# Performance work log

Measured on AMD Instinct MI355X. Metric: run time of the kernel, lower is better.

## Reference

```python
import jax, jax.numpy as jnp
import numpy as np

I_, J_, D_IN, D_H = 100, 8, 768, 64
N_NODES, N_HE, N_INC, N_CELLS, VOCAB = 160000, 320000, 1600000, 800, 30000
BN_EPS = 1e-5


def setup_inputs() -> dict:
    key = jax.random.key(0)
    ks = jax.random.split(key, 20)
    w = lambda k, s: jax.random.normal(k, s, jnp.float32) * 0.05
    inp = {}
    inp['x'] = jax.random.normal(ks[0], (I_, J_, D_IN), jnp.float32)
    inp['node_tokens'] = jax.random.randint(ks[1], (N_NODES,), 0, VOCAB)
    inp['inc_node'] = jax.random.randint(ks[2], (N_INC,), 0, N_NODES)
    inp['inc_hedge'] = jnp.sort(jax.random.randint(ks[3], (N_INC,), 0, N_HE))
    inp['node2cell'] = jnp.sort(jax.random.randint(ks[4], (N_NODES,), 0, N_CELLS))
    inp['vac_emb'] = w(ks[5], (VOCAB, D_IN))
    inp['fhi_w'] = w(ks[6], (D_IN, D_H)); inp['fhi_b'] = jnp.zeros((D_H,), jnp.float32)
    inp['fin_w'] = w(ks[7], (D_IN, D_H)); inp['fin_b'] = jnp.zeros((D_H,), jnp.float32)
    inp['th1'] = w(ks[8], (D_H, D_H)); inp['b1'] = jnp.zeros((D_H,), jnp.float32)
    inp['th2'] = w(ks[9], (D_H, D_H)); inp['b2'] = jnp.zeros((D_H,), jnp.float32)
    for li, k in zip((1, 2, 3), (ks[10], ks[11], ks[12])):
        inp[f'wc{li}'] = w(k, (D_H, D_H, 3))
        inp[f'bc{li}'] = jnp.zeros((D_H,), jnp.float32)
        inp[f'g{li}'] = jnp.ones((D_H,), jnp.float32)
        inp[f'be{li}'] = jnp.zeros((D_H,), jnp.float32)
        inp[f'm{li}'] = jnp.zeros((D_H,), jnp.float32)
        inp[f'v{li}'] = jnp.ones((D_H,), jnp.float32)
    inp['fct_w'] = w(ks[13], (D_H, D_H)); inp['fct_b'] = jnp.zeros((D_H,), jnp.float32)
    return inp


def _inv_safe(c):
    return jnp.where(c > 0, 1.0 / jnp.maximum(c, 1.0), 0.0)


def _hconv(xf, inc_node, inc_hedge, theta, bias):
    # PyG HypergraphConv (no attention): D^{-1} H W B^{-1} H^T (X Theta) + bias
    xt = xf @ theta                                        # [N, D]
    ones = jnp.ones((inc_node.shape[0],), xt.dtype)
    deg_e = jax.ops.segment_sum(ones, inc_hedge, N_HE)     # B_e
    he = jax.ops.segment_sum(xt[inc_node], inc_hedge, N_HE) * _inv_safe(deg_e)[:, None]
    deg_v = jax.ops.segment_sum(ones, inc_node, N_NODES)   # D_v
    out = jax.ops.segment_sum(he[inc_hedge], inc_node, N_NODES) * _inv_safe(deg_v)[:, None]
    return out + bias


def _conv_bn(h, wc, bc, g, be, m, v):
    # Conv1d(k=3, pad=1) -> ReLU -> BatchNorm1d (inference stats); dropout is eval-mode identity
    h = jax.lax.conv_general_dilated(h, wc, (1,), [(1, 1)],
                                     dimension_numbers=('NCH', 'OIH', 'NCH')) + bc[None, :, None]
    h = jax.nn.relu(h)
    return (h - m[None, :, None]) * (g[None, :, None] / jnp.sqrt(v[None, :, None] + BN_EPS)) + be[None, :, None]


def _forward(x, node_tokens, inc_node, inc_hedge, node2cell, vac_emb, fhi_w, fhi_b,
             fin_w, fin_b, th1, b1, th2, b2, wc1, bc1, g1, be1, m1, v1,
             wc2, bc2, g2, be2, m2, v2, wc3, bc3, g3, be3, m3, v3, fct_w, fct_b):
    # x = fin(x)
    x0 = jnp.einsum('ijd,dh->ijh', x, fin_w) + fin_b       # [100, 8, 64]
    # node_features = fhi(graph_embedding[graph.x])  (gather-dominated)
    nf = vac_emb[node_tokens] @ fhi_w + fhi_b              # [N, 64]
    # two HypergraphConv layers with residuals (eval-mode dropout = identity)
    h1 = jax.nn.relu(_hconv(nf, inc_node, inc_hedge, th1, b1)) + nf
    gx = jax.nn.relu(_hconv(h1, inc_node, inc_hedge, th2, b2)) + nf
    # per-graph mean + max pooling (graph.batch is all-zero per graph => one vector per cell)
    cnt = jax.ops.segment_sum(jnp.ones((N_NODES,), gx.dtype), node2cell, N_CELLS)
    mean_p = jax.ops.segment_sum(gx, node2cell, N_CELLS) * _inv_safe(cnt)[:, None]
    max_p = jax.ops.segment_max(gx, node2cell, N_CELLS)
    max_p = jnp.where(cnt[:, None] > 0, max_p, 0.0)
    cell_emb = 0.5 * (mean_p + max_p)                      # [800, 64]
    x_upd = x0 + 0.3 * cell_emb.reshape(I_, J_, D_H)       # x[i,j] += 0.3*graph_emb
    h = jnp.transpose(x_upd, (0, 2, 1))                    # [100, 64, 8]
    h = _conv_bn(h, wc1, bc1, g1, be1, m1, v1)
    h = _conv_bn(h, wc2, bc2, g2, be2, m2, v2)
    h = _conv_bn(h, wc3, bc3, g3, be3, m3, v3)
    out2 = jnp.mean(h, axis=2) @ fct_w + fct_b             # [100, 64]
    return x_upd, out2


def reference(x, node_tokens, inc_node, inc_hedge, node2cell, vac_emb, fhi_w, fhi_b,
              fin_w, fin_b, th1, b1, th2, b2, wc1, bc1, g1, be1, m1, v1,
              wc2, bc2, g2, be2, m2, v2, wc3, bc3, g3, be3, m3, v3, fct_w, fct_b):
    return _forward(x, node_tokens, inc_node, inc_hedge, node2cell, vac_emb, fhi_w, fhi_b,
                    fin_w, fin_b, th1, b1, th2, b2, wc1, bc1, g1, be1, m1, v1,
                    wc2, bc2, g2, be2, m2, v2, wc3, bc3, g3, be3, m3, v3, fct_w, fct_b)
```

## Files before the change

### kernel.cpp

```cpp
#include <hip/hip_runtime.h>
#include <hip/hip_bf16.h>
#include <cstdint>
#include <cstddef>

#define I_      100
#define J_      8
#define D_IN    768
#define D_H     64
#define N_NODES 160000
#define N_HE    320000
#define N_INC   1600000
#define N_CELLS 800
#define VOCAB   30000

#define NRANGE   256
#define NPR      625
#define SLAB     8192
#define NCHUNK   1000
#define EPB      (N_INC / NCHUNK)

typedef unsigned short u16;
using short8 = __attribute__((ext_vector_type(8))) short;
using f32x4  = __attribute__((ext_vector_type(4))) float;

__device__ __forceinline__ float bf2f(u16 u) {
    union { uint32_t i; float f; } x; x.i = ((uint32_t)u) << 16; return x.f;
}
__device__ __forceinline__ u16 f2bf(float f) {
    union { float f; uint32_t i; } x; x.f = f;
    uint32_t b = x.i;
    b += 0x7FFFu + ((b >> 16) & 1u);
    return (u16)(b >> 16);
}
__device__ __forceinline__ float lo_bf(uint32_t u) {
    union { uint32_t i; float f; } x; x.i = u << 16; return x.f;
}
__device__ __forceinline__ float hi_bf(uint32_t u) {
    union { uint32_t i; float f; } x; x.i = u & 0xFFFF0000u; return x.f;
}
__device__ __forceinline__ uint32_t pack_bf2(float a, float b) {
    return (uint32_t)f2bf(a) | ((uint32_t)f2bf(b) << 16);
}

#define G_OFF_HE   (N_INC / 256)
#define G_OFF_CELL (N_NODES / 256)
#define G_CONV_BIG ((D_IN * 64) / 256)
#define G_CONV_SM  ((64 * 64) / 256)
#define G_KA       NCHUNK
#define G_KB1      256
#define G_KC       NCHUNK
#define G_KD       256
#define G_PGEMM    ((VOCAB + 63) / 64)
#define G_XT       (N_NODES / 64)
#define G_X0       ((I_ * J_ + 63) / 64)
#define G_HEDGE    (N_HE / 32)
#define G_NODE     (N_NODES / 32)
#define G_NXT      (N_NODES / 32)

__device__ __forceinline__ void dev_offsets(int bid, const int* __restrict__ sorted,
                                            int n, int nbins, int* __restrict__ off) {
    int i = bid * 256 + threadIdx.x;
    if (i >= n) return;
    int cur = sorted[i];
    int prev = (i == 0) ? -1 : sorted[i - 1];
    for (int b = prev + 1; b <= cur; ++b) off[b] = i;
    if (i == n - 1) {
        for (int b = cur + 1; b <= nbins; ++b) off[b] = n;
    }
}

__device__ __forceinline__ void dev_convT(int bid, const float* __restrict__ B,
                                          u16* __restrict__ Bt, int K) {
    int g = bid * 256 + threadIdx.x;
    if (g >= K * 64) return;
    int k = g >> 6, n = g & 63;
    Bt[(size_t)n * K + k] = f2bf(B[g]);
}

__device__ __forceinline__ void dev_ka(int bid, const int* __restrict__ inc_node,
                                       int* __restrict__ counts, int* __restrict__ lds) {
    int tid = threadIdx.x;
    lds[tid] = 0;
    __syncthreads();
    int s = bid * EPB, e = s + EPB;
    for (int i = s + tid; i < e; i += 256)
        atomicAdd(&lds[(unsigned)inc_node[i] / NPR], 1);
    __syncthreads();
    counts[bid * NRANGE + tid] = lds[tid];
}

__device__ __forceinline__ void dev_kb1(int r, const int* __restrict__ counts,
                                        int* __restrict__ chunk_off,
                                        int* __restrict__ range_total,
                                        int* __restrict__ lds) {
    int tid = threadIdx.x;
    int c0 = tid * 4;
    int v0 = (c0     < NCHUNK) ? counts[(c0    ) * NRANGE + r] : 0;
    int v1 = (c0 + 1 < NCHUNK) ? counts[(c0 + 1) * NRANGE + r] : 0;
    int v2 = (c0 + 2 < NCHUNK) ? counts[(c0 + 2) * NRANGE + r] : 0;
    int v3 = (c0 + 3 < NCHUNK) ? counts[(c0 + 3) * NRANGE + r] : 0;
    int s = v0 + v1 + v2 + v3;
    lds[tid] = s;
    __syncthreads();
    #pragma unroll
    for (int d = 1; d < 256; d <<= 1) {
        int t = (tid >= d) ? lds[tid - d] : 0;
        __syncthreads();
        lds[tid] += t;
        __syncthreads();
    }
    int run = lds[tid] - s;
    if (c0     < NCHUNK) { chunk_off[(c0    ) * NRANGE + r] = run; run += v0; }
    if (c0 + 1 < NCHUNK) { chunk_off[(c0 + 1) * NRANGE + r] = run; run += v1; }
    if (c0 + 2 < NCHUNK) { chunk_off[(c0 + 2) * NRANGE + r] = run; run += v2; }
    if (c0 + 3 < NCHUNK) { chunk_off[(c0 + 3) * NRANGE + r] = run; run += v3; }
    if (tid == 255) range_total[r] = lds[255];
}

__device__ __forceinline__ void dev_kc(int bid, const int* __restrict__ inc_node,
                                       const int* __restrict__ inc_hedge,
                                       const int* __restrict__ chunk_off,
                                       int2* __restrict__ bucket, int* __restrict__ lds) {
    int tid = threadIdx.x;
    int* co  = lds;
    int* cur = lds + 256;
    co[tid]  = tid * SLAB + chunk_off[bid * NRANGE + tid];
    cur[tid] = 0;
    __syncthreads();
    int s = bid * EPB, e = s + EPB;
    for (int i = s + tid; i < e; i += 256) {
        int v = inc_node[i];
        int h = inc_hedge[i];
        int rg = (unsigned)v / NPR;
        int rank = atomicAdd(&cur[rg], 1);
        bucket[co[rg] + rank] = make_int2(v, h);
    }
}

__device__ __forceinline__ void dev_kd(int r, const int2* __restrict__ bucket,
                                       const int* __restrict__ range_total,
                                       int* __restrict__ node_off, int* __restrict__ node_deg,
                                       int* __restrict__ csr, int* __restrict__ lds) {
    int tid = threadIdx.x;
    int* hist = lds;
    int* tsum = lds + 768;
    int* cur  = lds + 1024;
    for (int i = tid; i < 768; i += 256) { hist[i] = 0; cur[i] = 0; }
    __syncthreads();
    int lo = r * NPR;
    int pb = r * SLAB;
    int pe = pb + range_total[r];
    for (int i = pb + tid; i < pe; i += 256)
        atomicAdd(&hist[bucket[i].x - lo], 1);
    __syncthreads();
    int b3 = tid * 3;
    int a0 = hist[b3], a1 = hist[b3 + 1], a2 = hist[b3 + 2];
    int s = a0 + a1 + a2;
    tsum[tid] = s;
    __syncthreads();
    #pragma unroll
    for (int d = 1; d < 256; d <<= 1) {
        int t = (tid >= d) ? tsum[tid - d] : 0;
        __syncthreads();
        tsum[tid] += t;
        __syncthreads();
    }
    int excl = tsum[tid] - s;
    hist[b3]     = excl;
    hist[b3 + 1] = excl + a0;
    hist[b3 + 2] = excl + a0 + a1;
    __syncthreads();
    for (int v = tid; v < NPR; v += 256) {
        int h0 = hist[v];
        node_off[lo + v] = pb + h0;
        node_deg[lo + v] = hist[v + 1] - h0;
    }
    for (int i = pb + tid; i < pe; i += 256) {
        int2 p = bucket[i];
        int l = p.x - lo;
        int k = atomicAdd(&cur[l], 1);
        csr[pb + hist[l] + k] = p.y;
    }
}

template <int BF16_OUT, int GATHER, int KK>
__device__ __forceinline__ void dev_gemm_direct(int wid, const float* __restrict__ A,
                                                const int* __restrict__ tok,
                                                const u16* __restrict__ Bt,
                                                const float* __restrict__ bias,
                                                void* __restrict__ C, int M) {
    int lane = threadIdx.x & 63;
    int m16 = lane & 15, q = lane >> 4;
    int base = wid << 4;
    if (base >= M) return;
    int row = base + m16;
    const float* arow = GATHER ? (A + ((size_t)tok[row] << 6))
                               : (A + (size_t)row * KK);

    f32x4 acc0 = {0.f, 0.f, 0.f, 0.f};
    f32x4 acc1 = {0.f, 0.f, 0.f, 0.f};
    f32x4 acc2 = {0.f, 0.f, 0.f, 0.f};
    f32x4 acc3 = {0.f, 0.f, 0.f, 0.f};

    #pragma unroll 2
    for (int kt = 0; kt < KK; kt += 32) {
        const float* ap = arow + kt + q * 8;
        float4 av0 = *reinterpret_cast<const float4*>(ap);
        float4 av1 = *reinterpret_cast<const float4*>(ap + 4);
        short8 a;
        a[0] = (short)f2bf(av0.x); a[1] = (short)f2bf(av0.y);
        a[2] = (short)f2bf(av0.z); a[3] = (short)f2bf(av0.w);
        a[4] = (short)f2bf(av1.x); a[5] = (short)f2bf(av1.y);
        a[6] = (short)f2bf(av1.z); a[7] = (short)f2bf(av1.w);
        const u16* bp = Bt + (size_t)m16 * KK + kt + q * 8;
        short8 b0 = *reinterpret_cast<const short8*>(bp);
        short8 b1 = *reinterpret_cast<const short8*>(bp + (size_t)16 * KK);
        short8 b2 = *reinterpret_cast<const short8*>(bp + (size_t)32 * KK);
        short8 b3 = *reinterpret_cast<const short8*>(bp + (size_t)48 * KK);
        acc0 = __builtin_amdgcn_mfma_f32_16x16x32_bf16(a, b0, acc0, 0, 0, 0);
        acc1 = __builtin_amdgcn_mfma_f32_16x16x32_bf16(a, b1, acc1, 0, 0, 0);
        acc2 = __builtin_amdgcn_mfma_f32_16x16x32_bf16(a, b2, acc2, 0, 0, 0);
        acc3 = __builtin_amdgcn_mfma_f32_16x16x32_bf16(a, b3, acc3, 0, 0, 0);
    }

    f32x4 accs[4] = {acc0, acc1, acc2, acc3};
    #pragma unroll
    for (int r = 0; r < 4; ++r) {
        int gr = base + q * 4 + r;
        #pragma unroll
        for (int j = 0; j < 4; ++j) {
            int col = j * 16 + m16;
            float v = accs[j][r];
            if (!BF16_OUT) v += bias[col];
            if (BF16_OUT)
                ((u16*)C)[(size_t)gr * 64 + col] = f2bf(v);
            else
                ((float*)C)[(size_t)gr * 64 + col] = v;
        }
    }
}

__device__ __forceinline__ void dev_hedge_sum(int bid, const int* __restrict__ inc_node,
                                              const int* __restrict__ he_off,
                                              const u16* __restrict__ xt,
                                              u16* __restrict__ he) {
    int w = (bid * 256 + (int)threadIdx.x) >> 6;
    int lane = threadIdx.x & 63;
    int sub = lane >> 3;
    int c8 = (lane & 7) << 3;
    int hedge = w * 8 + sub;
    if (hedge >= N_HE) return;
    int s = he_off[hedge], e = he_off[hedge + 1];

    float a0 = 0.f, a1 = 0.f, a2 = 0.f, a3 = 0.f;
    float a4 = 0.f, a5 = 0.f, a6 = 0.f, a7 = 0.f;
    float b0 = 0.f, b1 = 0.f, b2 = 0.f, b3 = 0.f;
    float b4 = 0.f, b5 = 0.f, b6 = 0.f, b7 = 0.f;

    int j = s;
    if ((e - s) & 1) {
        uint4 d = *reinterpret_cast<const uint4*>(xt + (((size_t)inc_node[j]) << 6) + c8);
        a0 += lo_bf(d.x); a1 += hi_bf(d.x);
        a2 += lo_bf(d.y); a3 += hi_bf(d.y);
        a4 += lo_bf(d.z); a5 += hi_bf(d.z);
        a6 += lo_bf(d.w); a7 += hi_bf(d.w);
        ++j;
    }
    int i0 = 0, i1 = 0;
    if (j < e) { i0 = inc_node[j]; i1 = inc_node[j + 1]; }
    for (; j < e; j += 2) {
        int c0 = i0, c1 = i1;
        if (j + 2 < e) { i0 = inc_node[j + 2]; i1 = inc_node[j + 3]; }
        uint4 d0 = *reinterpret_cast<const uint4*>(xt + (((size_t)c0) << 6) + c8);
        uint4 d1 = *reinterpret_cast<const uint4*>(xt + (((size_t)c1) << 6) + c8);
        a0 += lo_bf(d0.x); a1 += hi_bf(d0.x);
        a2 += lo_bf(d0.y); a3 += hi_bf(d0.y);
        a4 += lo_bf(d0.z); a5 += hi_bf(d0.z);
        a6 += lo_bf(d0.w); a7 += hi_bf(d0.w);
        b0 += lo_bf(d1.x); b1 += hi_bf(d1.x);
        b2 += lo_bf(d1.y); b3 += hi_bf(d1.y);
        b4 += lo_bf(d1.z); b5 += hi_bf(d1.z);
        b6 += lo_bf(d1.w); b7 += hi_bf(d1.w);
    }
    a0 += b0; a1 += b1; a2 += b2; a3 += b3;
    a4 += b4; a5 += b5; a6 += b6; a7 += b7;

    float inv = (e > s) ? 1.f / (float)(e - s) : 0.f;
    uint4 o;
    o.x = pack_bf2(a0 * inv, a1 * inv);
    o.y = pack_bf2(a2 * inv, a3 * inv);
    o.z = pack_bf2(a4 * inv, a5 * inv);
    o.w = pack_bf2(a6 * inv, a7 * inv);
    *reinterpret_cast<uint4*>(he + (((size_t)hedge) << 6) + c8) = o;
}

__device__ __forceinline__ void dev_node_core(int node, const int* __restrict__ csr,
                                              const int* __restrict__ node_off,
                                              const int* __restrict__ node_deg,
                                              const u16* __restrict__ he,
                                              const float* __restrict__ bias,
                                              const float* __restrict__ P,
                                              const int* __restrict__ tok,
                                              int c8, float* __restrict__ o) {
    int s = node_off[node];
    int e = s + node_deg[node];

    float a0 = 0.f, a1 = 0.f, a2 = 0.f, a3 = 0.f;
    float a4 = 0.f, a5 = 0.f, a6 = 0.f, a7 = 0.f;
    float b0 = 0.f, b1 = 0.f, b2 = 0.f, b3 = 0.f;
    float b4 = 0.f, b5 = 0.f, b6 = 0.f, b7 = 0.f;

    int j = s;
    if ((e - s) & 1) {
        uint4 d = *reinterpret_cast<const uint4*>(he + (((size_t)csr[j]) << 6) + c8);
        a0 += lo_bf(d.x); a1 += hi_bf(d.x);
        a2 += lo_bf(d.y); a3 += hi_bf(d.y);
        a4 += lo_bf(d.z); a5 += hi_bf(d.z);
        a6 += lo_bf(d.w); a7 += hi_bf(d.w);
        ++j;
    }
    int i0 = 0, i1 = 0;
    if (j < e) { i0 = csr[j]; i1 = csr[j + 1]; }
    for (; j < e; j += 2) {
        int c0 = i0, c1 = i1;
        if (j + 2 < e) { i0 = csr[j + 2]; i1 = csr[j + 3]; }
        uint4 d0 = *reinterpret_cast<const uint4*>(he + (((size_t)c0) << 6) + c8);
        uint4 d1 = *reinterpret_cast<const uint4*>(he + (((size_t)c1) << 6) + c8);
        a0 += lo_bf(d0.x); a1 += hi_bf(d0.x);
        a2 += lo_bf(d0.y); a3 += hi_bf(d0.y);
        a4 += lo_bf(d0.z); a5 += hi_bf(d0.z);
        a6 += lo_bf(d0.w); a7 += hi_bf(d0.w);
        b0 += lo_bf(d1.x); b1 += hi_bf(d1.x);
        b2 += lo_bf(d1.y); b3 += hi_bf(d1.y);
        b4 += lo_bf(d1.z); b5 += hi_bf(d1.z);
        b6 += lo_bf(d1.w); b7 += hi_bf(d1.w);
    }
    a0 += b0; a1 += b1; a2 += b2; a3 += b3;
    a4 += b4; a5 += b5; a6 += b6; a7 += b7;

    float inv = (e > s) ? 1.f / (float)(e - s) : 0.f;
    const float* nfp = P + (((size_t)tok[node]) << 6) + c8;
    float4 nv0 = *reinterpret_cast<const float4*>(nfp);
    float4 nv1 = *reinterpret_cast<const float4*>(nfp + 4);
    o[0] = fmaxf(fmaf(a0, inv, bias[c8 + 0]), 0.f) + nv0.x;
    o[1] = fmaxf(fmaf(a1, inv, bias[c8 + 1]), 0.f) + nv0.y;
    o[2] = fmaxf(fmaf(a2, inv, bias[c8 + 2]), 0.f) + nv0.z;
    o[3] = fmaxf(fmaf(a3, inv, bias[c8 + 3]), 0.f) + nv0.w;
    o[4] = fmaxf(fmaf(a4, inv, bias[c8 + 4]), 0.f) + nv1.x;
    o[5] = fmaxf(fmaf(a5, inv, bias[c8 + 5]), 0.f) + nv1.y;
    o[6] = fmaxf(fmaf(a6, inv, bias[c8 + 6]), 0.f) + nv1.z;
    o[7] = fmaxf(fmaf(a7, inv, bias[c8 + 7]), 0.f) + nv1.w;
}

__global__ __launch_bounds__(256) void k_node_xt(const int* __restrict__ csr,
                                                 const int* __restrict__ node_off,
                                                 const int* __restrict__ node_deg,
                                                 const u16* __restrict__ he,
                                                 const float* __restrict__ bias,
                                                 const float* __restrict__ P,
                                                 const int* __restrict__ tok,
                                                 const u16* __restrict__ Bt,
                                                 u16* __restrict__ xt) {
    __shared__ u16 h1s[32][72];
    int tid = threadIdx.x;
    int w = tid >> 6;
    int lane = tid & 63;
    int sub = lane >> 3;
    int c8 = (lane & 7) << 3;
    int rowib = w * 8 + sub;
    int node = blockIdx.x * 32 + rowib;

    float o[8];
    dev_node_core(node, csr, node_off, node_deg, he, bias, P, tok, c8, o);

    uint4 pk;
    pk.x = pack_bf2(o[0], o[1]);
    pk.y = pack_bf2(o[2], o[3]);
    pk.z = pack_bf2(o[4], o[5]);
    pk.w = pack_bf2(o[6], o[7]);
    *reinterpret_cast<uint4*>(&h1s[rowib][c8]) = pk;
    __syncthreads();

    if (w < 2) {
        int m16 = lane & 15, q = lane >> 4;
        int base = w * 16;
        f32x4 acc0 = {0.f, 0.f, 0.f, 0.f};
        f32x4 acc1 = {0.f, 0.f, 0.f, 0.f};
        f32x4 acc2 = {0.f, 0.f, 0.f, 0.f};
        f32x4 acc3 = {0.f, 0.f, 0.f, 0.f};
        #pragma unroll
        for (int kt = 0; kt < 64; kt += 32) {
            short8 a = *reinterpret_cast<const short8*>(&h1s[base + m16][kt + q * 8]);
            const u16* bp = Bt + (size_t)m16 * 64 + kt + q * 8;
            short8 b0 = *reinterpret_cast<const short8*>(bp);
            short8 b1 = *reinterpret_cast<const short8*>(bp + (size_t)16 * 64);
            short8 b2 = *reinterpret_cast<const short8*>(bp + (size_t)32 * 64);
            short8 b3 = *reinterpret_cast<const short8*>(bp + (size_t)48 * 64);
            acc0 = __builtin_amdgcn_mfma_f32_16x16x32_bf16(a, b0, acc0, 0, 0, 0);
            acc1 = __builtin_amdgcn_mfma_f32_16x16x32_bf16(a, b1, acc1, 0, 0, 0);
            acc2 = __builtin_amdgcn_mfma_f32_16x16x32_bf16(a, b2, acc2, 0, 0, 0);
            acc3 = __builtin_amdgcn_mfma_f32_16x16x32_bf16(a, b3, acc3, 0, 0, 0);
        }
        f32x4 accs[4] = {acc0, acc1, acc2, acc3};
        #pragma unroll
        for (int r = 0; r < 4; ++r) {
            int gr = blockIdx.x * 32 + base + q * 4 + r;
            #pragma unroll
            for (int jj = 0; jj < 4; ++jj) {
                int col = jj * 16 + m16;
                xt[(size_t)gr * 64 + col] = f2bf(accs[jj][r]);
            }
        }
    }
}

__global__ __launch_bounds__(256) void k_node_sum(const int* __restrict__ csr,
                                                  const int* __restrict__ node_off,
                                                  const int* __restrict__ node_deg,
                                                  const u16* __restrict__ he,
                                                  const float* __restrict__ bias,
                                                  const float* __restrict__ P,
                                                  const int* __restrict__ tok,
                                                  float* __restrict__ out) {
    int w = (blockIdx.x * 256 + (int)threadIdx.x) >> 6;
    int lane = threadIdx.x & 63;
    int sub = lane >> 3;
    int c8 = (lane & 7) << 3;
    int node = w * 8 + sub;
    if (node >= N_NODES) return;
    float o[8];
    dev_node_core(node, csr, node_off, node_deg, he, bias, P, tok, c8, o);
    float* op = out + (((size_t)node) << 6) + c8;
    float4 o0 = make_float4(o[0], o[1], o[2], o[3]);
    float4 o1 = make_float4(o[4], o[5], o[6], o[7]);
    *reinterpret_cast<float4*>(op) = o0;
    *reinterpret_cast<float4*>(op + 4) = o1;
}

__global__ __launch_bounds__(256) void k_p0(const float* __restrict__ fhi_w,
                                            const float* __restrict__ fin_w,
                                            const float* __restrict__ th1,
                                            const float* __restrict__ th2,
                                            u16* __restrict__ Bt_fhi, u16* __restrict__ Bt_fin,
                                            u16* __restrict__ Bt_th1, u16* __restrict__ Bt_th2,
                                            const int* __restrict__ inc_node,
                                            int* __restrict__ counts) {
    __shared__ int lds[256];
    int bid = blockIdx.x;
    if (bid < G_KA) { dev_ka(bid, inc_node, counts, lds); return; }
    bid -= G_KA;
    if (bid < G_CONV_BIG) { dev_convT(bid, fhi_w, Bt_fhi, D_IN); return; }
    bid -= G_CONV_BIG;
    if (bid < G_CONV_BIG) { dev_convT(bid, fin_w, Bt_fin, D_IN); return; }
    bid -= G_CONV_BIG;
    if (bid < G_CONV_SM) { dev_convT(bid, th1, Bt_th1, 64); return; }
    bid -= G_CONV_SM;
    dev_convT(bid, th2, Bt_th2, 64);
}

__global__ __launch_bounds__(256) void k_p1(const float* __restrict__ vac_emb,
                                            const u16* __restrict__ Bt_fhi,
                                            const float* __restrict__ fhi_b, float* __restrict__ P,
                                            const int* __restrict__ counts,
                                            int* __restrict__ chunk_off, int* __restrict__ range_total,
                                            const int* __restrict__ inc_hedge,
                                            const int* __restrict__ node2cell,
                                            int* __restrict__ he_off, int* __restrict__ cell_off) {
    __shared__ int lds[256];
    int bid = blockIdx.x;
    if (bid < G_KB1) { dev_kb1(bid, counts, chunk_off, range_total, lds); return; }
    bid -= G_KB1;
    if (bid < G_PGEMM) {
        int wid = bid * 4 + ((int)threadIdx.x >> 6);
        dev_gemm_direct<0, 0, D_IN>(wid, vac_emb, nullptr, Bt_fhi, fhi_b, P, VOCAB);
        return;
    }
    bid -= G_PGEMM;
    if (bid < G_OFF_HE) { dev_offsets(bid, inc_hedge, N_INC, N_HE, he_off); return; }
    bid -= G_OFF_HE;
    dev_offsets(bid, node2cell, N_NODES, N_CELLS, cell_off);
}

__global__ __launch_bounds__(256) void k_p2(const float* __restrict__ P,
                                            const int* __restrict__ tok,
                                            const u16* __restrict__ Bt_th1, u16* __restrict__ xt,
                                            const float* __restrict__ x, const u16* __restrict__ Bt_fin,
                                            const float* __restrict__ fin_b, float* __restrict__ x0,
                                            const int* __restrict__ inc_node,
                                            const int* __restrict__ inc_hedge,
                                            const int* __restrict__ chunk_off,
                                            int2* __restrict__ bucket) {
    __shared__ int lds[512];
    int bid = blockIdx.x;
    if (bid < G_KC) { dev_kc(bid, inc_node, inc_hedge, chunk_off, bucket, lds); return; }
    bid -= G_KC;
    if (bid < G_XT) {
        int wid = bid * 4 + ((int)threadIdx.x >> 6);
        dev_gemm_direct<1, 1, 64>(wid, P, tok, Bt_th1, nullptr, xt, N_NODES);
        return;
    }
    bid -= G_XT;
    {
        int wid = bid * 4 + ((int)threadIdx.x >> 6);
        dev_gemm_direct<0, 0, D_IN>(wid, x, nullptr, Bt_fin, fin_b, x0, I_ * J_);
    }
}

__global__ __launch_bounds__(256) void k_p3(const int* __restrict__ inc_node,
                                            const int* __restrict__ he_off,
                                            const u16* __restrict__ xt, u16* __restrict__ he,
                                            const int2* __restrict__ bucket,
                                            const int* __restrict__ range_total,
                                            int* __restrict__ node_off, int* __restrict__ node_deg,
                                            int* __restrict__ csr) {
    __shared__ int lds[1792];
    int bid = blockIdx.x;
    if (bid < G_KD) { dev_kd(bid, bucket, range_total, node_off, node_deg, csr, lds); return; }
    bid -= G_KD;
    dev_hedge_sum(bid, inc_node, he_off, xt, he);
}

__global__ __launch_bounds__(256) void k_hedge_sum(const int* __restrict__ inc_node,
                                                   const int* __restrict__ he_off,
                                                   const u16* __restrict__ xt,
                                                   u16* __restrict__ he) {
    dev_hedge_sum(blockIdx.x, inc_node, he_off, xt, he);
}

__global__ __launch_bounds__(256) void k_pool(const float* __restrict__ gx,
                                              const int* __restrict__ cell_off,
                                              const float* __restrict__ x0,
                                              float* __restrict__ out1) {
    __shared__ float ssum[4][64];
    __shared__ float smax[4][64];
    int c = blockIdx.x;
    int lane = threadIdx.x & 63;
    int w = threadIdx.x >> 6;
    int s = cell_off[c], e = cell_off[c + 1];
    float sum = 0.f, mx = -INFINITY;
    for (int n = s + w; n < e; n += 4) {
        float v = gx[((size_t)n << 6) + lane];
        sum += v;
        mx = fmaxf(mx, v);
    }
    ssum[w][lane] = sum;
    smax[w][lane] = mx;
    __syncthreads();
    if (w == 0) {
        sum = ssum[0][lane] + ssum[1][lane] + ssum[2][lane] + ssum[3][lane];
        mx = fmaxf(fmaxf(smax[0][lane], smax[1][lane]), fmaxf(smax[2][lane], smax[3][lane]));
        int cnt = e - s;
        float mean = (cnt > 0) ? sum / (float)cnt : 0.f;
        float mp = (cnt > 0) ? mx : 0.f;
        float ce = 0.5f * (mean + mp);
        out1[((size_t)c << 6) + lane] = x0[((size_t)c << 6) + lane] + 0.3f * ce;
    }
}

__global__ __launch_bounds__(256) void k_tcn(
    const float* __restrict__ xu,
    const float* __restrict__ wc1, const float* __restrict__ bc1, const float* __restrict__ g1,
    const float* __restrict__ be1, const float* __restrict__ m1, const float* __restrict__ v1,
    const float* __restrict__ wc2, const float* __restrict__ bc2, const float* __restrict__ g2,
    const float* __restrict__ be2, const float* __restrict__ m2, const float* __restrict__ v2,
    const float* __restrict__ wc3, const float* __restrict__ bc3, const float* __restrict__ g3,
    const float* __restrict__ be3, const float* __restrict__ m3, const float* __restrict__ v3,
    const float* __restrict__ fct_w, const float* __restrict__ fct_b,
    float* __restrict__ out2) {
    __shared__ float w_lds[64 * 64 * 3];
    __shared__ float hA[64][10];
    __shared__ float hB[64][10];
    __shared__ float mo[64];

    int n = blockIdx.x, tid = threadIdx.x;

    if (tid < 64) {
        hA[tid][0] = 0.f; hA[tid][9] = 0.f;
        hB[tid][0] = 0.f; hB[tid][9] = 0.f;
    }
    #pragma unroll
    for (int l = tid; l < 512; l += 256) {
        int t = l >> 6, i = l & 63;
        hA[i][t + 1] = xu[(size_t)n * 512 + l];
    }

    const float* wcs[3] = {wc1, wc2, wc3};
    const float* bcs[3] = {bc1, bc2, bc3};
    const float* gs[3]  = {g1, g2, g3};
    const float* bes[3] = {be1, be2, be3};
    const float* ms[3]  = {m1, m2, m3};
    const float* vs[3]  = {v1, v2, v3};

    float (*hin)[10] = hA;
    float (*hout)[10] = hB;

    #pragma unroll
    for (int li = 0; li < 3; ++li) {
        for (int l = tid; l < 64 * 64 * 3; l += 256) w_lds[l] = wcs[li][l];
        __syncthreads();
        #pragma unroll
        for (int rep = 0; rep < 2; ++rep) {
            int idx = tid + rep * 256;
            int o = idx >> 3, t = idx & 7;
            float acc = bcs[li][o];
            #pragma unroll 8
            for (int i = 0; i < 64; ++i) {
                const float* wr = &w_lds[o * 192 + i * 3];
                acc = fmaf(hin[i][t + 0], wr[0], acc);
                acc = fmaf(hin[i][t + 1], wr[1], acc);
                acc = fmaf(hin[i][t + 2], wr[2], acc);
            }
            acc = fmaxf(acc, 0.f);
            float sc = gs[li][o] * rsqrtf(vs[li][o] + 1e-5f);
            acc = (acc - ms[li][o]) * sc + bes[li][o];
            hout[o][t + 1] = acc;
        }
        __syncthreads();
        float (*tmp)[10] = hin; hin = hout; hout = tmp;
    }

    if (tid < 64) {
        float s = 0.f;
        #pragma unroll
        for (int t = 0; t < 8; ++t) s += hin[tid][t + 1];
        mo[tid] = s * 0.125f;
    }
    __syncthreads();
    if (tid < 64) {
        float acc = fct_b[tid];
        #pragma unroll 8
        for (int o = 0; o < 64; ++o) acc = fmaf(mo[o], fct_w[o * 64 + tid], acc);
        out2[(size_t)n * 64 + tid] = acc;
    }
}

extern "C" void kernel_launch(void* const* d_in, const int* in_sizes, int n_in,
                              void* d_out, int out_size, void* d_ws, size_t ws_size,
                              hipStream_t stream) {
    (void)in_sizes; (void)n_in; (void)out_size; (void)ws_size;

    const float* x          = (const float*)d_in[0];
    const int*   node_tok   = (const int*)d_in[1];
    const int*   inc_node   = (const int*)d_in[2];
    const int*   inc_hedge  = (const int*)d_in[3];
    const int*   node2cell  = (const int*)d_in[4];
    const float* vac_emb    = (const float*)d_in[5];
    const float* fhi_w      = (const float*)d_in[6];
    const float* fhi_b      = (const float*)d_in[7];
    const float* fin_w      = (const float*)d_in[8];
    const float* fin_b      = (const float*)d_in[9];
    const float* th1        = (const float*)d_in[10];
    const float* b1         = (const float*)d_in[11];
    const float* th2        = (const float*)d_in[12];
    const float* b2         = (const float*)d_in[13];
    const float* fct_w      = (const float*)d_in[32];
    const float* fct_b      = (const float*)d_in[33];

    char* ws = (char*)d_ws;
    size_t off = 0;
    float* P        = (float*)(ws + off); off += (size_t)VOCAB * 64 * 4;
    float* hbuf     = (float*)(ws + off); off += (size_t)N_NODES * 64 * 4;
    u16*   xt       = (u16*)(ws + off);   off += (size_t)N_NODES * 64 * 2;
    u16*   he       = (u16*)(ws + off);   off += (size_t)N_HE * 64 * 2;
    int2*  bucket   = (int2*)(ws + off);  off += (size_t)NRANGE * SLAB * 8;
    int*   csr      = (int*)(ws + off);   off += (size_t)NRANGE * SLAB * 4;
    float* x0       = (float*)(ws + off); off += (size_t)N_CELLS * 64 * 4;
    u16*   Bt_fhi   = (u16*)(ws + off);   off += (size_t)64 * D_IN * 2;
    u16*   Bt_fin   = (u16*)(ws + off);   off += (size_t)64 * D_IN * 2;
    u16*   Bt_th1   = (u16*)(ws + off);   off += (size_t)64 * 64 * 2;
    u16*   Bt_th2   = (u16*)(ws + off);   off += (size_t)64 * 64 * 2;
    int*   he_off   = (int*)(ws + off);   off += ((size_t)(N_HE + 1) * 4 + 255) / 256 * 256;
    int*   node_off = (int*)(ws + off);   off += (size_t)N_NODES * 4;
    int*   node_deg = (int*)(ws + off);   off += (size_t)N_NODES * 4;
    int*   cell_off = (int*)(ws + off);   off += ((size_t)(N_CELLS + 1) * 4 + 255) / 256 * 256;

    int*  counts      = (int*)hbuf;
    int*  chunk_off   = counts + NCHUNK * NRANGE;
    int*  range_total = chunk_off + NCHUNK * NRANGE;

    float* out1 = (float*)d_out;
    float* out2 = out1 + (size_t)I_ * J_ * D_H;

    k_p0<<<G_KA + 2 * G_CONV_BIG + 2 * G_CONV_SM, 256, 0, stream>>>(
        fhi_w, fin_w, th1, th2, Bt_fhi, Bt_fin, Bt_th1, Bt_th2,
        inc_node, counts);

    k_p1<<<G_KB1 + G_PGEMM + G_OFF_HE + G_OFF_CELL, 256, 0, stream>>>(
        vac_emb, Bt_fhi, fhi_b, P, counts, chunk_off, range_total,
        inc_hedge, node2cell, he_off, cell_off);

    k_p2<<<G_KC + G_XT + G_X0, 256, 0, stream>>>(
        P, node_tok, Bt_th1, xt, x, Bt_fin, fin_b, x0,
        inc_node, inc_hedge, chunk_off, bucket);

    k_p3<<<G_KD + G_HEDGE, 256, 0, stream>>>(inc_node, he_off, xt, he,
                                             bucket, range_total, node_off, node_deg, csr);

    k_node_xt<<<G_NXT, 256, 0, stream>>>(csr, node_off, node_deg, he, b1, P, node_tok,
                                         Bt_th2, xt);

    k_hedge_sum<<<G_HEDGE, 256, 0, stream>>>(inc_node, he_off, xt, he);

    k_node_sum<<<G_NODE, 256, 0, stream>>>(csr, node_off, node_deg, he, b2, P, node_tok, hbuf);

    k_pool<<<N_CELLS, 256, 0, stream>>>(hbuf, cell_off, x0, out1);

    k_tcn<<<I_, 256, 0, stream>>>(out1,
        (const float*)d_in[14], (const float*)d_in[15], (const float*)d_in[16],
        (const float*)d_in[17], (const float*)d_in[18], (const float*)d_in[19],
        (const float*)d_in[20], (const float*)d_in[21], (const float*)d_in[22],
        (const float*)d_in[23], (const float*)d_in[24], (const float*)d_in[25],
        (const float*)d_in[26], (const float*)d_in[27], (const float*)d_in[28],
        (const float*)d_in[29], (const float*)d_in[30], (const float*)d_in[31],
        fct_w, fct_b, out2);
}
```

Before: 484.3 us.

## Precompute theta1 projection per vocab token and gather through token ids

The first hypergraph conv's X·Theta1 was computed per node (160k rows gathered from the vocab table). Since node features are just vocab embeddings, the GEMM is now applied to the 30k-row vocab projection table, and the hyperedge sum gathers through node_tokens into that table. This shrinks the GEMM work and removes the per-node xt write. In exchange, the gather in the hyperedge sum adds an extra level of indirection through the token array.

```diff
diff --git a/kernel.cpp b/kernel.cpp
--- a/kernel.cpp
+++ b/kernel.cpp
@@ -51,7 +51,7 @@
 #define G_KC       NCHUNK
 #define G_KD       256
 #define G_PGEMM    ((VOCAB + 63) / 64)
-#define G_XT       (N_NODES / 64)
+#define G_PT1      ((VOCAB + 63) / 64)
 #define G_X0       ((I_ * J_ + 63) / 64)
 #define G_HEDGE    (N_HE / 32)
 #define G_NODE     (N_NODES / 32)
@@ -240,9 +240,11 @@
     }
 }
 
+template <int TOK>
 __device__ __forceinline__ void dev_hedge_sum(int bid, const int* __restrict__ inc_node,
                                               const int* __restrict__ he_off,
-                                              const u16* __restrict__ xt,
+                                              const u16* __restrict__ src,
+                                              const int* __restrict__ tok,
                                               u16* __restrict__ he) {
     int w = (bid * 256 + (int)threadIdx.x) >> 6;
     int lane = threadIdx.x & 63;
@@ -259,20 +261,30 @@
 
     int j = s;
     if ((e - s) & 1) {
-        uint4 d = *reinterpret_cast<const uint4*>(xt + (((size_t)inc_node[j]) << 6) + c8);
+        int v = inc_node[j];
+        int r = TOK ? tok[v] : v;
+        uint4 d = *reinterpret_cast<const uint4*>(src + (((size_t)r) << 6) + c8);
         a0 += lo_bf(d.x); a1 += hi_bf(d.x);
         a2 += lo_bf(d.y); a3 += hi_bf(d.y);
         a4 += lo_bf(d.z); a5 += hi_bf(d.z);
         a6 += lo_bf(d.w); a7 += hi_bf(d.w);
         ++j;
     }
-    int i0 = 0, i1 = 0;
-    if (j < e) { i0 = inc_node[j]; i1 = inc_node[j + 1]; }
+    int r0 = 0, r1 = 0;
+    if (j < e) {
+        int va = inc_node[j], vb = inc_node[j + 1];
+        r0 = TOK ? tok[va] : va;
+        r1 = TOK ? tok[vb] : vb;
+    }
     for (; j < e; j += 2) {
-        int c0 = i0, c1 = i1;
-        if (j + 2 < e) { i0 = inc_node[j + 2]; i1 = inc_node[j + 3]; }
-        uint4 d0 = *reinterpret_cast<const uint4*>(xt + (((size_t)c0) << 6) + c8);
-        uint4 d1 = *reinterpret_cast<const uint4*>(xt + (((size_t)c1) << 6) + c8);
+        int c0 = r0, c1 = r1;
+        if (j + 2 < e) {
+            int va = inc_node[j + 2], vb = inc_node[j + 3];
+            r0 = TOK ? tok[va] : va;
+            r1 = TOK ? tok[vb] : vb;
+        }
+        uint4 d0 = *reinterpret_cast<const uint4*>(src + (((size_t)c0) << 6) + c8);
+        uint4 d1 = *reinterpret_cast<const uint4*>(src + (((size_t)c1) << 6) + c8);
         a0 += lo_bf(d0.x); a1 += hi_bf(d0.x);
         a2 += lo_bf(d0.y); a3 += hi_bf(d0.y);
         a4 += lo_bf(d0.z); a5 += hi_bf(d0.z);
@@ -482,8 +494,7 @@
 }
 
 __global__ __launch_bounds__(256) void k_p2(const float* __restrict__ P,
-                                            const int* __restrict__ tok,
-                                            const u16* __restrict__ Bt_th1, u16* __restrict__ xt,
+                                            const u16* __restrict__ Bt_th1, u16* __restrict__ PT1,
                                             const float* __restrict__ x, const u16* __restrict__ Bt_fin,
                                             const float* __restrict__ fin_b, float* __restrict__ x0,
                                             const int* __restrict__ inc_node,
@@ -494,12 +505,12 @@
     int bid = blockIdx.x;
     if (bid < G_KC) { dev_kc(bid, inc_node, inc_hedge, chunk_off, bucket, lds); return; }
     bid -= G_KC;
-    if (bid < G_XT) {
+    if (bid < G_PT1) {
         int wid = bid * 4 + ((int)threadIdx.x >> 6);
-        dev_gemm_direct<1, 1, 64>(wid, P, tok, Bt_th1, nullptr, xt, N_NODES);
+        dev_gemm_direct<1, 0, 64>(wid, P, nullptr, Bt_th1, nullptr, PT1, VOCAB);
         return;
     }
-    bid -= G_XT;
+    bid -= G_PT1;
     {
         int wid = bid * 4 + ((int)threadIdx.x >> 6);
         dev_gemm_direct<0, 0, D_IN>(wid, x, nullptr, Bt_fin, fin_b, x0, I_ * J_);
@@ -508,7 +519,9 @@
 
 __global__ __launch_bounds__(256) void k_p3(const int* __restrict__ inc_node,
                                             const int* __restrict__ he_off,
-                                            const u16* __restrict__ xt, u16* __restrict__ he,
+                                            const u16* __restrict__ PT1,
+                                            const int* __restrict__ tok,
+                                            u16* __restrict__ he,
                                             const int2* __restrict__ bucket,
                                             const int* __restrict__ range_total,
                                             int* __restrict__ node_off, int* __restrict__ node_deg,
@@ -517,14 +530,14 @@
     int bid = blockIdx.x;
     if (bid < G_KD) { dev_kd(bid, bucket, range_total, node_off, node_deg, csr, lds); return; }
     bid -= G_KD;
-    dev_hedge_sum(bid, inc_node, he_off, xt, he);
+    dev_hedge_sum<1>(bid, inc_node, he_off, PT1, tok, he);
 }
 
 __global__ __launch_bounds__(256) void k_hedge_sum(const int* __restrict__ inc_node,
                                                    const int* __restrict__ he_off,
                                                    const u16* __restrict__ xt,
                                                    u16* __restrict__ he) {
-    dev_hedge_sum(blockIdx.x, inc_node, he_off, xt, he);
+    dev_hedge_sum<0>(blockIdx.x, inc_node, he_off, xt, nullptr, he);
 }
 
 __global__ __launch_bounds__(256) void k_pool(const float* __restrict__ gx,
@@ -673,6 +686,7 @@
     int*   node_off = (int*)(ws + off);   off += (size_t)N_NODES * 4;
     int*   node_deg = (int*)(ws + off);   off += (size_t)N_NODES * 4;
     int*   cell_off = (int*)(ws + off);   off += ((size_t)(N_CELLS + 1) * 4 + 255) / 256 * 256;
+    u16*   PT1      = (u16*)(ws + off);   off += (size_t)VOCAB * 64 * 2;
 
     int*  counts      = (int*)hbuf;
     int*  chunk_off   = counts + NCHUNK * NRANGE;
@@ -689,11 +703,11 @@
         vac_emb, Bt_fhi, fhi_b, P, counts, chunk_off, range_total,
         inc_hedge, node2cell, he_off, cell_off);
 
-    k_p2<<<G_KC + G_XT + G_X0, 256, 0, stream>>>(
-        P, node_tok, Bt_th1, xt, x, Bt_fin, fin_b, x0,
+    k_p2<<<G_KC + G_PT1 + G_X0, 256, 0, stream>>>(
+        P, Bt_th1, PT1, x, Bt_fin, fin_b, x0,
         inc_node, inc_hedge, chunk_off, bucket);
 
-    k_p3<<<G_KD + G_HEDGE, 256, 0, stream>>>(inc_node, he_off, xt, he,
+    k_p3<<<G_KD + G_HEDGE, 256, 0, stream>>>(inc_node, he_off, PT1, node_tok, he,
                                              bucket, range_total, node_off, node_deg, csr);
 
     k_node_xt<<<G_NXT, 256, 0, stream>>>(csr, node_off, node_deg, he, b1, P, node_tok,
```

Result: faster. 473.9 us (-2.1%).
